# Kernel optimization log

Hardware: AMD Instinct MI355X
Metric: run time of the kernel (lower is better)

Reference implementation:

```python
import jax, jax.numpy as jnp
import numpy as np

N_NODES = 50000
N_EDGES = 800000
NUM_GRAPHS = 128

def _sage_conv(x, src, dst, Wl, b, Wr):
    # PyG SAGEConv: lin_l(mean_{j in N(i)} x_j) + lin_r(x_i); bias only on lin_l
    msgs = x[src]                                             # [E, d] gather
    agg = jax.ops.segment_sum(msgs, dst, num_segments=N_NODES)
    deg = jax.ops.segment_sum(jnp.ones((src.shape[0],), x.dtype), dst,
                              num_segments=N_NODES)
    mean = agg / jnp.maximum(deg, 1.0)[:, None]               # [N, d]
    return mean @ Wl.T + b + x @ Wr.T

def setup_inputs() -> dict:
    key = jax.random.key(0)
    ks = jax.random.split(key, 12)
    d_in, d_h, d_out = 96, 96, 64
    def w(k, o, i):
        return jax.random.normal(k, (o, i), jnp.float32) * (1.0 / np.sqrt(i))
    return {
        "x": jax.random.normal(ks[0], (N_NODES, d_in), jnp.float32),
        "edge_index": jax.random.randint(ks[1], (2, N_EDGES), 0, N_NODES, jnp.int32),
        "batch": jnp.sort(jax.random.randint(ks[2], (N_NODES,), 0, NUM_GRAPHS, jnp.int32)),
        "Wl0": w(ks[3], d_h, d_in), "b0": jnp.zeros((d_h,), jnp.float32), "Wr0": w(ks[4], d_h, d_in),
        "Wl1": w(ks[5], d_h, d_h),  "b1": jnp.zeros((d_h,), jnp.float32), "Wr1": w(ks[6], d_h, d_h),
        "Wl2": w(ks[7], d_out, d_h), "b2": jnp.zeros((d_out,), jnp.float32), "Wr2": w(ks[8], d_out, d_h),
    }

def reference(x, edge_index, batch, Wl0, b0, Wr0, Wl1, b1, Wr1, Wl2, b2, Wr2):
    src, dst = edge_index[0], edge_index[1]
    h = jax.nn.relu(_sage_conv(x, src, dst, Wl0, b0, Wr0))   # dropout: eval mode -> identity
    h = jax.nn.relu(_sage_conv(h, src, dst, Wl1, b1, Wr1))
    h = _sage_conv(h, src, dst, Wl2, b2, Wr2)                 # [N, out]
    # global_mean_pool over graphs
    pooled = jax.ops.segment_sum(h, batch, num_segments=NUM_GRAPHS)
    cnt = jax.ops.segment_sum(jnp.ones((h.shape[0],), h.dtype), batch,
                              num_segments=NUM_GRAPHS)
    return pooled / jnp.maximum(cnt, 1.0)[:, None]            # [num_graphs, out]
```

## Files before the change

kernel.cpp:

```cpp
#include <hip/hip_runtime.h>
#include <stdint.h>
#include <stddef.h>

#define NN 50000
#define NP 50048
#define NE 800000
#define NG 128

#define NBKT 256
#define NPB 196
#define BCAP 4096
#define TILE_E 3072
#define PARTB 261
#define AGB 3125
#define TFB 782

typedef __attribute__((ext_vector_type(8))) short bf16x8;
typedef __attribute__((ext_vector_type(4))) float f32x4;
typedef __attribute__((ext_vector_type(4))) unsigned int u32x4;
typedef unsigned short ushort_t;
typedef unsigned int uint_t;

static __device__ inline ushort_t f2b(float f) {
    union { float f; uint_t u; } v; v.f = f;
    uint_t r = v.u + 0x7FFFu + ((v.u >> 16) & 1u);
    return (ushort_t)(r >> 16);
}
static __device__ inline float blo(uint_t u) {
    union { uint_t u; float f; } v; v.u = u << 16; return v.f;
}
static __device__ inline float bhi(uint_t u) {
    union { uint_t u; float f; } v; v.u = u & 0xFFFF0000u; return v.f;
}

__launch_bounds__(256) static __global__
void part_zero_kernel(const int* __restrict__ src, const int* __restrict__ dst,
                      int* __restrict__ bucket_cnt, uint_t* __restrict__ part,
                      float* __restrict__ accum) {
    __shared__ int hist[NBKT];
    int tid = threadIdx.x;
    if (blockIdx.x < PARTB) {
        hist[tid] = 0;
        __syncthreads();
        int base = blockIdx.x * TILE_E;
        int end = min(base + TILE_E, NE);
        for (int i = base + tid; i < end; i += 256)
            atomicAdd(&hist[dst[i] / NPB], 1);
        __syncthreads();
        int r = atomicAdd(&bucket_cnt[tid], hist[tid]);
        __syncthreads();
        hist[tid] = r;
        __syncthreads();
        for (int i = base + tid; i < end; i += 256) {
            int s = src[i], d = dst[i];
            int b = d / NPB;
            int dl = d - b * NPB;
            int p = atomicAdd(&hist[b], 1);
            part[b * BCAP + p] = ((uint_t)dl << 16) | (uint_t)s;
        }
    } else {
        int gid = (blockIdx.x - PARTB) * 256 + tid;
        if (gid < NG * 64) accum[gid] = 0.f;
    }
}

static __device__ void csr_build_body(int b, char* smem, const uint_t* __restrict__ part,
                                      const int* __restrict__ bucket_cnt, int* __restrict__ deg,
                                      int* __restrict__ offs, int* __restrict__ csr) {
    uint_t* stage = (uint_t*)smem;
    ushort_t* cstage = (ushort_t*)(smem + 16384);
    int* cnt_s = (int*)(smem + 24576);
    int* scan_l = (int*)(smem + 25600);
    int* cur_l = (int*)(smem + 26624);
    int tid = threadIdx.x;
    int bc = bucket_cnt[tid];
    cnt_s[tid] = bc;
    scan_l[tid] = bc;
    __syncthreads();
    for (int off = 1; off < NBKT; off <<= 1) {
        int t = (tid >= off) ? scan_l[tid - off] : 0;
        __syncthreads();
        scan_l[tid] += t;
        __syncthreads();
    }
    int base = scan_l[b] - cnt_s[b];
    int n = cnt_s[b];
    __syncthreads();
    cnt_s[tid] = 0;
    __syncthreads();
    for (int i = tid; i < n; i += 256) {
        uint_t e = part[(size_t)b * BCAP + i];
        stage[i] = e;
        atomicAdd(&cnt_s[e >> 16], 1);
    }
    __syncthreads();
    int v = cnt_s[tid];
    scan_l[tid] = v;
    __syncthreads();
    for (int off = 1; off < NBKT; off <<= 1) {
        int t = (tid >= off) ? scan_l[tid - off] : 0;
        __syncthreads();
        scan_l[tid] += t;
        __syncthreads();
    }
    int ex = scan_l[tid] - v;
    scan_l[tid] = ex;
    cur_l[tid] = 0;
    __syncthreads();
    int g = b * NPB + tid;
    if (tid < NPB && g < NN) { deg[g] = v; offs[g] = base + ex; }
    for (int i = tid; i < n; i += 256) {
        uint_t e = stage[i];
        int dl = e >> 16;
        int p = atomicAdd(&cur_l[dl], 1);
        cstage[scan_l[dl] + p] = (ushort_t)(e & 0xFFFFu);
    }
    __syncthreads();
    for (int i = tid; i < n; i += 256) csr[base + i] = (int)cstage[i];
}

template <int DOUT, int NT, bool FP32_IN>
static __device__ void transform_body(int bid, char* smem,
                                      const void* __restrict__ hin, const float* __restrict__ Wl,
                                      const float* __restrict__ bias, const float* __restrict__ Wr,
                                      ushort_t* __restrict__ tlc, ushort_t* __restrict__ trc) {
    constexpr int DIN = 96;
    short* w_s = (short*)smem;
    int tid = threadIdx.x;
    for (int idx = tid; idx < NT * 3 * 64; idx += 256) {
        int ci = idx >> 6, ln = idx & 63;
        int t = ci / 3, s = ci - 3 * t;
        int o = t * 16 + (ln & 15);
        int c0 = s * 32 + (ln >> 4) * 8;
        const float* wrow = (o < DOUT) ? (Wl + (size_t)o * DIN)
                                       : (Wr + (size_t)(o - DOUT) * DIN);
        float4 v0 = *(const float4*)(wrow + c0);
        float4 v1 = *(const float4*)(wrow + c0 + 4);
        bf16x8 pk;
        pk[0] = (short)f2b(v0.x); pk[1] = (short)f2b(v0.y);
        pk[2] = (short)f2b(v0.z); pk[3] = (short)f2b(v0.w);
        pk[4] = (short)f2b(v1.x); pk[5] = (short)f2b(v1.y);
        pk[6] = (short)f2b(v1.z); pk[7] = (short)f2b(v1.w);
        *(bf16x8*)&w_s[idx * 8] = pk;
    }
    int lane = tid & 63;
    int m0 = bid * 64 + (tid >> 6) * 16;
    int row = m0 + (lane & 15);
    bf16x8 a0, a1, a2;
    if (FP32_IN) {
        const float* xr = (const float*)hin + (size_t)min(row, NN - 1) * DIN + (lane >> 4) * 8;
#pragma unroll
        for (int s = 0; s < 3; s++) {
            float4 v0 = *(const float4*)(xr + s * 32);
            float4 v1 = *(const float4*)(xr + s * 32 + 4);
            bf16x8 pk;
            pk[0] = (short)f2b(v0.x); pk[1] = (short)f2b(v0.y);
            pk[2] = (short)f2b(v0.z); pk[3] = (short)f2b(v0.w);
            pk[4] = (short)f2b(v1.x); pk[5] = (short)f2b(v1.y);
            pk[6] = (short)f2b(v1.z); pk[7] = (short)f2b(v1.w);
            if (s == 0) a0 = pk; else if (s == 1) a1 = pk; else a2 = pk;
        }
    } else {
        const bf16x8* arow = (const bf16x8*)((const ushort_t*)hin + (size_t)row * DIN) + (lane >> 4);
        a0 = arow[0];
        a1 = arow[4];
        a2 = arow[8];
    }
    __syncthreads();
    const bf16x8* wp = (const bf16x8*)w_s + lane;
    f32x4 acc[NT];
#pragma unroll
    for (int t = 0; t < NT; t++) {
        acc[t] = (f32x4){0.f, 0.f, 0.f, 0.f};
        acc[t] = __builtin_amdgcn_mfma_f32_16x16x32_bf16(a0, wp[(t * 3 + 0) * 64], acc[t], 0, 0, 0);
        acc[t] = __builtin_amdgcn_mfma_f32_16x16x32_bf16(a1, wp[(t * 3 + 1) * 64], acc[t], 0, 0, 0);
        acc[t] = __builtin_amdgcn_mfma_f32_16x16x32_bf16(a2, wp[(t * 3 + 2) * 64], acc[t], 0, 0, 0);
    }
    int quad = lane >> 4, col = lane & 15;
#pragma unroll
    for (int t = 0; t < NT; t++) {
        int o = t * 16 + col;
        bool is_r = (o >= DOUT);
        float bv = is_r ? bias[o - DOUT] : 0.f;
        ushort_t* outp = is_r ? trc : tlc;
        int oo = is_r ? (o - DOUT) : o;
        int cch = oo >> 5, f = oo & 31;
        ushort_t* ob = outp + ((size_t)cch * NN) * 32 + f;
#pragma unroll
        for (int r = 0; r < 4; r++) {
            int node = m0 + quad * 4 + r;
            if (node < NN) ob[(size_t)node * 32] = f2b(acc[t][r] + bv);
        }
    }
}

__launch_bounds__(256) static __global__
void csr_tf0_kernel(const uint_t* __restrict__ part, const int* __restrict__ bucket_cnt,
                    int* __restrict__ deg, int* __restrict__ offs, int* __restrict__ csr,
                    const float* __restrict__ x, const float* __restrict__ Wl0,
                    const float* __restrict__ b0, const float* __restrict__ Wr0,
                    ushort_t* __restrict__ tlc, ushort_t* __restrict__ trc) {
    __shared__ __align__(16) char smem[36864];
    if (blockIdx.x < NBKT)
        csr_build_body(blockIdx.x, smem, part, bucket_cnt, deg, offs, csr);
    else
        transform_body<96, 12, true>(blockIdx.x - NBKT, smem, x, Wl0, b0, Wr0, tlc, trc);
}

template <int DOUT, int NT>
__launch_bounds__(256, 4) static __global__
void transform_kernel(const ushort_t* __restrict__ hb, const float* __restrict__ Wl,
                      const float* __restrict__ bias, const float* __restrict__ Wr,
                      ushort_t* __restrict__ tlc, ushort_t* __restrict__ trc) {
    __shared__ __align__(16) char smem[NT * 3 * 64 * 8 * 2];
    transform_body<DOUT, NT, false>(blockIdx.x, smem, hb, Wl, bias, Wr, tlc, trc);
}

template <int D>
__launch_bounds__(256) static __global__
void agg3_kernel(const ushort_t* __restrict__ tlc, const ushort_t* __restrict__ trc,
                 const int* __restrict__ offs, const int* __restrict__ deg,
                 const int* __restrict__ csr, ushort_t* __restrict__ outb) {
    int bx = blockIdx.x;
    int c = bx / AGB;
    int b = bx - c * AGB;
    int tid = threadIdx.x;
    int node = b * 16 + (tid >> 4);
    int lane = tid & 15;
    int ng = lane >> 2, fl = lane & 3;
    const uint_t* tl = (const uint_t*)tlc + (size_t)c * NN * 16;
    int off = offs[node], dg = deg[node];
    float acc[8];
#pragma unroll
    for (int q = 0; q < 8; q++) acc[q] = 0.f;
    int k = 0;
    for (; k + 8 <= dg; k += 8) {
        int s0 = csr[off + k + ng];
        int s1 = csr[off + k + 4 + ng];
        uint4 a0 = *(const uint4*)(tl + (size_t)s0 * 16 + 4 * fl);
        uint4 a1 = *(const uint4*)(tl + (size_t)s1 * 16 + 4 * fl);
        acc[0] += blo(a0.x) + blo(a1.x); acc[1] += bhi(a0.x) + bhi(a1.x);
        acc[2] += blo(a0.y) + blo(a1.y); acc[3] += bhi(a0.y) + bhi(a1.y);
        acc[4] += blo(a0.z) + blo(a1.z); acc[5] += bhi(a0.z) + bhi(a1.z);
        acc[6] += blo(a0.w) + blo(a1.w); acc[7] += bhi(a0.w) + bhi(a1.w);
    }
    if (k + 4 <= dg) {
        int s0 = csr[off + k + ng];
        uint4 a0 = *(const uint4*)(tl + (size_t)s0 * 16 + 4 * fl);
        acc[0] += blo(a0.x); acc[1] += bhi(a0.x);
        acc[2] += blo(a0.y); acc[3] += bhi(a0.y);
        acc[4] += blo(a0.z); acc[5] += bhi(a0.z);
        acc[6] += blo(a0.w); acc[7] += bhi(a0.w);
        k += 4;
    }
    if (ng < dg - k) {
        int s0 = csr[off + k + ng];
        uint4 a0 = *(const uint4*)(tl + (size_t)s0 * 16 + 4 * fl);
        acc[0] += blo(a0.x); acc[1] += bhi(a0.x);
        acc[2] += blo(a0.y); acc[3] += bhi(a0.y);
        acc[4] += blo(a0.z); acc[5] += bhi(a0.z);
        acc[6] += blo(a0.w); acc[7] += bhi(a0.w);
    }
#pragma unroll
    for (int q = 0; q < 8; q++) {
        acc[q] += __shfl_xor(acc[q], 4, 64);
        acc[q] += __shfl_xor(acc[q], 8, 64);
    }
    float s = 1.f / (float)max(dg, 1);
    u32x4 t = __builtin_nontemporal_load(
        (const u32x4*)((const uint_t*)trc + (size_t)c * NN * 16 + (size_t)node * 16 + 4 * fl));
    float v0 = fmaxf(fmaf(acc[0], s, blo(t.x)), 0.f);
    float v1 = fmaxf(fmaf(acc[1], s, bhi(t.x)), 0.f);
    float v2 = fmaxf(fmaf(acc[2], s, blo(t.y)), 0.f);
    float v3 = fmaxf(fmaf(acc[3], s, bhi(t.y)), 0.f);
    float v4 = fmaxf(fmaf(acc[4], s, blo(t.z)), 0.f);
    float v5 = fmaxf(fmaf(acc[5], s, bhi(t.z)), 0.f);
    float v6 = fmaxf(fmaf(acc[6], s, blo(t.w)), 0.f);
    float v7 = fmaxf(fmaf(acc[7], s, bhi(t.w)), 0.f);
    if (ng == 0) {
        u32x4 o;
        o.x = (uint_t)f2b(v0) | ((uint_t)f2b(v1) << 16);
        o.y = (uint_t)f2b(v2) | ((uint_t)f2b(v3) << 16);
        o.z = (uint_t)f2b(v4) | ((uint_t)f2b(v5) << 16);
        o.w = (uint_t)f2b(v6) | ((uint_t)f2b(v7) << 16);
        __builtin_nontemporal_store(
            o, (u32x4*)((uint_t*)outb + (size_t)node * (D / 2) + c * 16 + 4 * fl));
    }
}

__launch_bounds__(256) static __global__
void agg_pool_kernel(const ushort_t* __restrict__ tlc, const ushort_t* __restrict__ trc,
                     const int* __restrict__ offs, const int* __restrict__ deg,
                     const int* __restrict__ csr, const int* __restrict__ batch,
                     float* __restrict__ accum) {
    __shared__ float hsum[16][32];
    __shared__ int gids[16];
    int bx = blockIdx.x;
    int c = bx / AGB;
    int b = bx - c * AGB;
    int tid = threadIdx.x;
    int nl = tid >> 4;
    int node = b * 16 + nl;
    int lane = tid & 15;
    int ng = lane >> 2, fl = lane & 3;
    if (tid < 16) gids[tid] = batch[b * 16 + tid];
    const uint_t* tl = (const uint_t*)tlc + (size_t)c * NN * 16;
    int off = offs[node], dg = deg[node];
    float acc[8];
#pragma unroll
    for (int q = 0; q < 8; q++) acc[q] = 0.f;
    int k = 0;
    for (; k + 8 <= dg; k += 8) {
        int s0 = csr[off + k + ng];
        int s1 = csr[off + k + 4 + ng];
        uint4 a0 = *(const uint4*)(tl + (size_t)s0 * 16 + 4 * fl);
        uint4 a1 = *(const uint4*)(tl + (size_t)s1 * 16 + 4 * fl);
        acc[0] += blo(a0.x) + blo(a1.x); acc[1] += bhi(a0.x) + bhi(a1.x);
        acc[2] += blo(a0.y) + blo(a1.y); acc[3] += bhi(a0.y) + bhi(a1.y);
        acc[4] += blo(a0.z) + blo(a1.z); acc[5] += bhi(a0.z) + bhi(a1.z);
        acc[6] += blo(a0.w) + blo(a1.w); acc[7] += bhi(a0.w) + bhi(a1.w);
    }
    if (k + 4 <= dg) {
        int s0 = csr[off + k + ng];
        uint4 a0 = *(const uint4*)(tl + (size_t)s0 * 16 + 4 * fl);
        acc[0] += blo(a0.x); acc[1] += bhi(a0.x);
        acc[2] += blo(a0.y); acc[3] += bhi(a0.y);
        acc[4] += blo(a0.z); acc[5] += bhi(a0.z);
        acc[6] += blo(a0.w); acc[7] += bhi(a0.w);
        k += 4;
    }
    if (ng < dg - k) {
        int s0 = csr[off + k + ng];
        uint4 a0 = *(const uint4*)(tl + (size_t)s0 * 16 + 4 * fl);
        acc[0] += blo(a0.x); acc[1] += bhi(a0.x);
        acc[2] += blo(a0.y); acc[3] += bhi(a0.y);
        acc[4] += blo(a0.z); acc[5] += bhi(a0.z);
        acc[6] += blo(a0.w); acc[7] += bhi(a0.w);
    }
#pragma unroll
    for (int q = 0; q < 8; q++) {
        acc[q] += __shfl_xor(acc[q], 4, 64);
        acc[q] += __shfl_xor(acc[q], 8, 64);
    }
    float s = 1.f / (float)max(dg, 1);
    u32x4 t = __builtin_nontemporal_load(
        (const u32x4*)((const uint_t*)trc + (size_t)c * NN * 16 + (size_t)node * 16 + 4 * fl));
    if (ng == 0) {
        hsum[nl][8 * fl + 0] = fmaf(acc[0], s, blo(t.x));
        hsum[nl][8 * fl + 1] = fmaf(acc[1], s, bhi(t.x));
        hsum[nl][8 * fl + 2] = fmaf(acc[2], s, blo(t.y));
        hsum[nl][8 * fl + 3] = fmaf(acc[3], s, bhi(t.y));
        hsum[nl][8 * fl + 4] = fmaf(acc[4], s, blo(t.z));
        hsum[nl][8 * fl + 5] = fmaf(acc[5], s, bhi(t.z));
        hsum[nl][8 * fl + 6] = fmaf(acc[6], s, blo(t.w));
        hsum[nl][8 * fl + 7] = fmaf(acc[7], s, bhi(t.w));
    }
    __syncthreads();
    if (tid < 32) {
        int gcur = gids[0];
        float ps = 0.f;
        for (int j = 0; j < 16; j++) {
            int g = gids[j];
            if (g != gcur) {
                atomicAdd(&accum[gcur * 64 + c * 32 + tid], ps);
                ps = 0.f; gcur = g;
            }
            ps += hsum[j][tid];
        }
        atomicAdd(&accum[gcur * 64 + c * 32 + tid], ps);
    }
}

__launch_bounds__(256) static __global__
void finalize_kernel(const float* __restrict__ accum, const int* __restrict__ batch,
                     float* __restrict__ out) {
    int i = blockIdx.x * 256 + threadIdx.x;
    if (i >= NG * 64) return;
    int g = i >> 6;
    int lo = 0, hi = NN;
    while (lo < hi) { int mid = (lo + hi) >> 1; if (batch[mid] < g) lo = mid + 1; else hi = mid; }
    int start = lo;
    hi = NN;
    while (lo < hi) { int mid = (lo + hi) >> 1; if (batch[mid] < g + 1) lo = mid + 1; else hi = mid; }
    int cnt = lo - start;
    out[i] = accum[i] / (float)max(cnt, 1);
}

extern "C" void kernel_launch(void* const* d_in, const int* in_sizes, int n_in,
                              void* d_out, int out_size, void* d_ws, size_t ws_size,
                              hipStream_t stream) {
    (void)in_sizes; (void)n_in; (void)out_size; (void)ws_size;
    const float* x   = (const float*)d_in[0];
    const int*   ei  = (const int*)d_in[1];
    const int*   bat = (const int*)d_in[2];
    const float* Wl0 = (const float*)d_in[3];
    const float* b0  = (const float*)d_in[4];
    const float* Wr0 = (const float*)d_in[5];
    const float* Wl1 = (const float*)d_in[6];
    const float* b1  = (const float*)d_in[7];
    const float* Wr1 = (const float*)d_in[8];
    const float* Wl2 = (const float*)d_in[9];
    const float* b2  = (const float*)d_in[10];
    const float* Wr2 = (const float*)d_in[11];
    float* out = (float*)d_out;
    const int* src = ei;
    const int* dst = ei + NE;

    char* p = (char*)d_ws;
    auto carve = [&](size_t bytes) -> char* {
        char* r = p;
        p += (bytes + 255) & ~(size_t)255;
        return r;
    };
    int*      deg    = (int*)carve((size_t)NN * 4);
    int*      offs   = (int*)carve((size_t)NN * 4);
    int*      bucket_cnt = (int*)carve(NBKT * 4);
    uint_t*   part   = (uint_t*)carve((size_t)NBKT * BCAP * 4);
    int*      csr    = (int*)carve((size_t)NE * 4);
    float*    accum  = (float*)carve((size_t)NG * 64 * 4);
    ushort_t* h1b    = (ushort_t*)carve((size_t)NP * 96 * 2);
    ushort_t* h2b    = (ushort_t*)carve((size_t)NP * 96 * 2);
    ushort_t* tlc    = (ushort_t*)carve((size_t)3 * NN * 32 * 2);
    ushort_t* trc    = (ushort_t*)carve((size_t)3 * NN * 32 * 2);

    dim3 b256(256);
    hipMemsetAsync(bucket_cnt, 0, NBKT * 4, stream);

    part_zero_kernel<<<dim3(PARTB + 32), b256, 0, stream>>>(src, dst, bucket_cnt, part, accum);
    csr_tf0_kernel<<<dim3(NBKT + TFB), b256, 0, stream>>>(part, bucket_cnt, deg, offs, csr,
                                                          x, Wl0, b0, Wr0, tlc, trc);
    agg3_kernel<96><<<dim3(3 * AGB), b256, 0, stream>>>(tlc, trc, offs, deg, csr, h1b);
    transform_kernel<96, 12><<<dim3(TFB), b256, 0, stream>>>(h1b, Wl1, b1, Wr1, tlc, trc);
    agg3_kernel<96><<<dim3(3 * AGB), b256, 0, stream>>>(tlc, trc, offs, deg, csr, h2b);
    transform_kernel<64, 8><<<dim3(TFB), b256, 0, stream>>>(h2b, Wl2, b2, Wr2, tlc, trc);
    agg_pool_kernel<<<dim3(2 * AGB), b256, 0, stream>>>(tlc, trc, offs, deg, csr, bat, accum);
    finalize_kernel<<<dim3((NG * 64 + 255) / 256), b256, 0, stream>>>(accum, bat, out);
}
```

Measured before the change: 240.8 us.

## Fold pool finalize into aggregation, unroll gather deeper, halve partition tile

Removes the finalize kernel. Per-graph inverse counts are precomputed in the partition kernel's spare blocks, and the pooled sums are pre-scaled before atomically adding them straight into the output. The neighbor gather loop is unrolled to 16 edges per iteration to keep more loads in flight, and the edge-partition tile is halved to launch twice as many blocks. This saves a launch and adds memory-level parallelism, at the cost of more registers and more global atomics on the bucket counters.

```diff
diff --git a/kernel.cpp b/kernel.cpp
--- a/kernel.cpp
+++ b/kernel.cpp
@@ -10,8 +10,8 @@
 #define NBKT 256
 #define NPB 196
 #define BCAP 4096
-#define TILE_E 3072
-#define PARTB 261
+#define TILE_E 1536
+#define PARTB 521
 #define AGB 3125
 #define TFB 782
 
@@ -36,7 +36,8 @@
 __launch_bounds__(256) static __global__
 void part_zero_kernel(const int* __restrict__ src, const int* __restrict__ dst,
                       int* __restrict__ bucket_cnt, uint_t* __restrict__ part,
-                      float* __restrict__ accum) {
+                      float* __restrict__ out, const int* __restrict__ batch,
+                      float* __restrict__ inv_cnt) {
     __shared__ int hist[NBKT];
     int tid = threadIdx.x;
     if (blockIdx.x < PARTB) {
@@ -60,7 +61,16 @@
         }
     } else {
         int gid = (blockIdx.x - PARTB) * 256 + tid;
-        if (gid < NG * 64) accum[gid] = 0.f;
+        if (gid < NG * 64) out[gid] = 0.f;
+        if (gid < NG) {
+            int g = gid;
+            int lo = 0, hi = NN;
+            while (lo < hi) { int m = (lo + hi) >> 1; if (batch[m] < g) lo = m + 1; else hi = m; }
+            int start = lo;
+            hi = NN;
+            while (lo < hi) { int m = (lo + hi) >> 1; if (batch[m] < g + 1) lo = m + 1; else hi = m; }
+            inv_cnt[g] = 1.f / (float)max(lo - start, 1);
+        }
     }
 }
 
@@ -216,6 +226,59 @@
     transform_body<DOUT, NT, false>(blockIdx.x, smem, hb, Wl, bias, Wr, tlc, trc);
 }
 
+static __device__ inline void gather_accum(const uint_t* __restrict__ tl,
+                                           const int* __restrict__ csr,
+                                           int off, int dg, int ng, int fl,
+                                           float* __restrict__ acc) {
+    int k = 0;
+    for (; k + 16 <= dg; k += 16) {
+        int s0 = csr[off + k + ng];
+        int s1 = csr[off + k + 4 + ng];
+        int s2 = csr[off + k + 8 + ng];
+        int s3 = csr[off + k + 12 + ng];
+        uint4 a0 = *(const uint4*)(tl + (size_t)s0 * 16 + 4 * fl);
+        uint4 a1 = *(const uint4*)(tl + (size_t)s1 * 16 + 4 * fl);
+        uint4 a2 = *(const uint4*)(tl + (size_t)s2 * 16 + 4 * fl);
+        uint4 a3 = *(const uint4*)(tl + (size_t)s3 * 16 + 4 * fl);
+        acc[0] += (blo(a0.x) + blo(a1.x)) + (blo(a2.x) + blo(a3.x));
+        acc[1] += (bhi(a0.x) + bhi(a1.x)) + (bhi(a2.x) + bhi(a3.x));
+        acc[2] += (blo(a0.y) + blo(a1.y)) + (blo(a2.y) + blo(a3.y));
+        acc[3] += (bhi(a0.y) + bhi(a1.y)) + (bhi(a2.y) + bhi(a3.y));
+        acc[4] += (blo(a0.z) + blo(a1.z)) + (blo(a2.z) + blo(a3.z));
+        acc[5] += (bhi(a0.z) + bhi(a1.z)) + (bhi(a2.z) + bhi(a3.z));
+        acc[6] += (blo(a0.w) + blo(a1.w)) + (blo(a2.w) + blo(a3.w));
+        acc[7] += (bhi(a0.w) + bhi(a1.w)) + (bhi(a2.w) + bhi(a3.w));
+    }
+    if (k + 8 <= dg) {
+        int s0 = csr[off + k + ng];
+        int s1 = csr[off + k + 4 + ng];
+        uint4 a0 = *(const uint4*)(tl + (size_t)s0 * 16 + 4 * fl);
+        uint4 a1 = *(const uint4*)(tl + (size_t)s1 * 16 + 4 * fl);
+        acc[0] += blo(a0.x) + blo(a1.x); acc[1] += bhi(a0.x) + bhi(a1.x);
+        acc[2] += blo(a0.y) + blo(a1.y); acc[3] += bhi(a0.y) + bhi(a1.y);
+        acc[4] += blo(a0.z) + blo(a1.z); acc[5] += bhi(a0.z) + bhi(a1.z);
+        acc[6] += blo(a0.w) + blo(a1.w); acc[7] += bhi(a0.w) + bhi(a1.w);
+        k += 8;
+    }
+    if (k + 4 <= dg) {
+        int s0 = csr[off + k + ng];
+        uint4 a0 = *(const uint4*)(tl + (size_t)s0 * 16 + 4 * fl);
+        acc[0] += blo(a0.x); acc[1] += bhi(a0.x);
+        acc[2] += blo(a0.y); acc[3] += bhi(a0.y);
+        acc[4] += blo(a0.z); acc[5] += bhi(a0.z);
+        acc[6] += blo(a0.w); acc[7] += bhi(a0.w);
+        k += 4;
+    }
+    if (ng < dg - k) {
+        int s0 = csr[off + k + ng];
+        uint4 a0 = *(const uint4*)(tl + (size_t)s0 * 16 + 4 * fl);
+        acc[0] += blo(a0.x); acc[1] += bhi(a0.x);
+        acc[2] += blo(a0.y); acc[3] += bhi(a0.y);
+        acc[4] += blo(a0.z); acc[5] += bhi(a0.z);
+        acc[6] += blo(a0.w); acc[7] += bhi(a0.w);
+    }
+}
+
 template <int D>
 __launch_bounds__(256) static __global__
 void agg3_kernel(const ushort_t* __restrict__ tlc, const ushort_t* __restrict__ trc,
@@ -233,34 +296,7 @@
     float acc[8];
 #pragma unroll
     for (int q = 0; q < 8; q++) acc[q] = 0.f;
-    int k = 0;
-    for (; k + 8 <= dg; k += 8) {
-        int s0 = csr[off + k + ng];
-        int s1 = csr[off + k + 4 + ng];
-        uint4 a0 = *(const uint4*)(tl + (size_t)s0 * 16 + 4 * fl);
-        uint4 a1 = *(const uint4*)(tl + (size_t)s1 * 16 + 4 * fl);
-        acc[0] += blo(a0.x) + blo(a1.x); acc[1] += bhi(a0.x) + bhi(a1.x);
-        acc[2] += blo(a0.y) + blo(a1.y); acc[3] += bhi(a0.y) + bhi(a1.y);
-        acc[4] += blo(a0.z) + blo(a1.z); acc[5] += bhi(a0.z) + bhi(a1.z);
-        acc[6] += blo(a0.w) + blo(a1.w); acc[7] += bhi(a0.w) + bhi(a1.w);
-    }
-    if (k + 4 <= dg) {
-        int s0 = csr[off + k + ng];
-        uint4 a0 = *(const uint4*)(tl + (size_t)s0 * 16 + 4 * fl);
-        acc[0] += blo(a0.x); acc[1] += bhi(a0.x);
-        acc[2] += blo(a0.y); acc[3] += bhi(a0.y);
-        acc[4] += blo(a0.z); acc[5] += bhi(a0.z);
-        acc[6] += blo(a0.w); acc[7] += bhi(a0.w);
-        k += 4;
-    }
-    if (ng < dg - k) {
-        int s0 = csr[off + k + ng];
-        uint4 a0 = *(const uint4*)(tl + (size_t)s0 * 16 + 4 * fl);
-        acc[0] += blo(a0.x); acc[1] += bhi(a0.x);
-        acc[2] += blo(a0.y); acc[3] += bhi(a0.y);
-        acc[4] += blo(a0.z); acc[5] += bhi(a0.z);
-        acc[6] += blo(a0.w); acc[7] += bhi(a0.w);
-    }
+    gather_accum(tl, csr, off, dg, ng, fl, acc);
 #pragma unroll
     for (int q = 0; q < 8; q++) {
         acc[q] += __shfl_xor(acc[q], 4, 64);
@@ -292,7 +328,7 @@
 void agg_pool_kernel(const ushort_t* __restrict__ tlc, const ushort_t* __restrict__ trc,
                      const int* __restrict__ offs, const int* __restrict__ deg,
                      const int* __restrict__ csr, const int* __restrict__ batch,
-                     float* __restrict__ accum) {
+                     const float* __restrict__ inv_cnt, float* __restrict__ out) {
     __shared__ float hsum[16][32];
     __shared__ int gids[16];
     int bx = blockIdx.x;
@@ -309,34 +345,7 @@
     float acc[8];
 #pragma unroll
     for (int q = 0; q < 8; q++) acc[q] = 0.f;
-    int k = 0;
-    for (; k + 8 <= dg; k += 8) {
-        int s0 = csr[off + k + ng];
-        int s1 = csr[off + k + 4 + ng];
-        uint4 a0 = *(const uint4*)(tl + (size_t)s0 * 16 + 4 * fl);
-        uint4 a1 = *(const uint4*)(tl + (size_t)s1 * 16 + 4 * fl);
-        acc[0] += blo(a0.x) + blo(a1.x); acc[1] += bhi(a0.x) + bhi(a1.x);
-        acc[2] += blo(a0.y) + blo(a1.y); acc[3] += bhi(a0.y) + bhi(a1.y);
-        acc[4] += blo(a0.z) + blo(a1.z); acc[5] += bhi(a0.z) + bhi(a1.z);
-        acc[6] += blo(a0.w) + blo(a1.w); acc[7] += bhi(a0.w) + bhi(a1.w);
-    }
-    if (k + 4 <= dg) {
-        int s0 = csr[off + k + ng];
-        uint4 a0 = *(const uint4*)(tl + (size_t)s0 * 16 + 4 * fl);
-        acc[0] += blo(a0.x); acc[1] += bhi(a0.x);
-        acc[2] += blo(a0.y); acc[3] += bhi(a0.y);
-        acc[4] += blo(a0.z); acc[5] += bhi(a0.z);
-        acc[6] += blo(a0.w); acc[7] += bhi(a0.w);
-        k += 4;
-    }
-    if (ng < dg - k) {
-        int s0 = csr[off + k + ng];
-        uint4 a0 = *(const uint4*)(tl + (size_t)s0 * 16 + 4 * fl);
-        acc[0] += blo(a0.x); acc[1] += bhi(a0.x);
-        acc[2] += blo(a0.y); acc[3] += bhi(a0.y);
-        acc[4] += blo(a0.z); acc[5] += bhi(a0.z);
-        acc[6] += blo(a0.w); acc[7] += bhi(a0.w);
-    }
+    gather_accum(tl, csr, off, dg, ng, fl, acc);
 #pragma unroll
     for (int q = 0; q < 8; q++) {
         acc[q] += __shfl_xor(acc[q], 4, 64);
@@ -362,28 +371,13 @@
         for (int j = 0; j < 16; j++) {
             int g = gids[j];
             if (g != gcur) {
-                atomicAdd(&accum[gcur * 64 + c * 32 + tid], ps);
+                atomicAdd(&out[gcur * 64 + c * 32 + tid], ps * inv_cnt[gcur]);
                 ps = 0.f; gcur = g;
             }
             ps += hsum[j][tid];
         }
-        atomicAdd(&accum[gcur * 64 + c * 32 + tid], ps);
-    }
-}
-
-__launch_bounds__(256) static __global__
-void finalize_kernel(const float* __restrict__ accum, const int* __restrict__ batch,
-                     float* __restrict__ out) {
-    int i = blockIdx.x * 256 + threadIdx.x;
-    if (i >= NG * 64) return;
-    int g = i >> 6;
-    int lo = 0, hi = NN;
-    while (lo < hi) { int mid = (lo + hi) >> 1; if (batch[mid] < g) lo = mid + 1; else hi = mid; }
-    int start = lo;
-    hi = NN;
-    while (lo < hi) { int mid = (lo + hi) >> 1; if (batch[mid] < g + 1) lo = mid + 1; else hi = mid; }
-    int cnt = lo - start;
-    out[i] = accum[i] / (float)max(cnt, 1);
+        atomicAdd(&out[gcur * 64 + c * 32 + tid], ps * inv_cnt[gcur]);
+    }
 }
 
 extern "C" void kernel_launch(void* const* d_in, const int* in_sizes, int n_in,
@@ -415,9 +409,9 @@
     int*      deg    = (int*)carve((size_t)NN * 4);
     int*      offs   = (int*)carve((size_t)NN * 4);
     int*      bucket_cnt = (int*)carve(NBKT * 4);
+    float*    inv_cnt = (float*)carve(NG * 4);
     uint_t*   part   = (uint_t*)carve((size_t)NBKT * BCAP * 4);
     int*      csr    = (int*)carve((size_t)NE * 4);
-    float*    accum  = (float*)carve((size_t)NG * 64 * 4);
     ushort_t* h1b    = (ushort_t*)carve((size_t)NP * 96 * 2);
     ushort_t* h2b    = (ushort_t*)carve((size_t)NP * 96 * 2);
     ushort_t* tlc    = (ushort_t*)carve((size_t)3 * NN * 32 * 2);
@@ -426,13 +420,14 @@
     dim3 b256(256);
     hipMemsetAsync(bucket_cnt, 0, NBKT * 4, stream);
 
-    part_zero_kernel<<<dim3(PARTB + 32), b256, 0, stream>>>(src, dst, bucket_cnt, part, accum);
+    part_zero_kernel<<<dim3(PARTB + 32), b256, 0, stream>>>(src, dst, bucket_cnt, part,
+                                                            out, bat, inv_cnt);
     csr_tf0_kernel<<<dim3(NBKT + TFB), b256, 0, stream>>>(part, bucket_cnt, deg, offs, csr,
                                                           x, Wl0, b0, Wr0, tlc, trc);
     agg3_kernel<96><<<dim3(3 * AGB), b256, 0, stream>>>(tlc, trc, offs, deg, csr, h1b);
     transform_kernel<96, 12><<<dim3(TFB), b256, 0, stream>>>(h1b, Wl1, b1, Wr1, tlc, trc);
     agg3_kernel<96><<<dim3(3 * AGB), b256, 0, stream>>>(tlc, trc, offs, deg, csr, h2b);
     transform_kernel<64, 8><<<dim3(TFB), b256, 0, stream>>>(h2b, Wl2, b2, Wr2, tlc, trc);
-    agg_pool_kernel<<<dim3(2 * AGB), b256, 0, stream>>>(tlc, trc, offs, deg, csr, bat, accum);
-    finalize_kernel<<<dim3((NG * 64 + 255) / 256), b256, 0, stream>>>(accum, bat, out);
-}
+    agg_pool_kernel<<<dim3(2 * AGB), b256, 0, stream>>>(tlc, trc, offs, deg, csr, bat,
+                                                        inv_cnt, out);
+}
```

After: 237.0 us. No clear change (-1.6%).
